# Kernel optimization log

Measured on AMD Instinct MI355X. Metric: run time of the kernel, lower is better.

Reference implementation:

```python
import jax, jax.numpy as jnp
import numpy as np

N_QUBITS = 8
N_LAYERS = 4


def _apply_1q(state, U, q):
    """Apply a 2x2 gate U (shape (2,2) shared, or (B,2,2) per-sample) on qubit q.
    state: (B, 2, 2, ..., 2) with qubit q on axis q+1 (wire 0 = most significant)."""
    a = q + 1
    st = jnp.moveaxis(state, a, -1)
    shp = st.shape
    st = st.reshape(shp[0], -1, 2)  # (B, rest, 2)
    if U.ndim == 3:
        st = jnp.einsum('bij,brj->bri', U, st)
    else:
        st = jnp.einsum('ij,brj->bri', U, st)
    return jnp.moveaxis(st.reshape(shp), -1, a)


def _cnot(state, c, t):
    ac, at = c + 1, t + 1
    s0 = jnp.take(state, 0, axis=ac)
    s1 = jnp.take(state, 1, axis=ac)
    at2 = at - 1 if at > ac else at  # axis shift after removing control axis
    s1 = jnp.flip(s1, axis=at2)      # X on target where control = 1
    return jnp.stack([s0, s1], axis=ac)


def _rx(t):
    c = jnp.cos(t / 2)
    s = jnp.sin(t / 2)
    return jnp.stack([jnp.stack([c + 0j, -1j * s]),
                      jnp.stack([-1j * s, c + 0j])]).astype(jnp.complex64)


def _ry(t):
    c = jnp.cos(t / 2)
    s = jnp.sin(t / 2)
    return jnp.stack([jnp.stack([c, -s]),
                      jnp.stack([s, c])]).astype(jnp.complex64)


def _rz(t):
    return jnp.diag(jnp.stack([jnp.exp(-1j * t / 2),
                               jnp.exp(1j * t / 2)])).astype(jnp.complex64)


def _ry_batched(t):
    # t: (B,) -> (B, 2, 2)
    c = jnp.cos(t / 2)
    s = jnp.sin(t / 2)
    U = jnp.stack([jnp.stack([c, -s], axis=-1),
                   jnp.stack([s, c], axis=-1)], axis=-2)
    return U.astype(jnp.complex64)


def setup_inputs() -> dict:
    key = jax.random.key(0)
    k1, k2 = jax.random.split(key)
    B = 16384
    x = jax.random.normal(k1, (B, N_QUBITS), dtype=jnp.float32)
    weights = jax.random.normal(k2, (N_QUBITS * N_LAYERS * 3,), dtype=jnp.float32) * 0.1
    return {"x": x, "weights": weights}


def reference(x, weights):
    n, L = N_QUBITS, N_LAYERS
    B = x.shape[0]
    state = jnp.zeros((B,) + (2,) * n, dtype=jnp.complex64)
    state = state.at[(slice(None),) + (0,) * n].set(1.0)

    # angle encoding: per-sample RY on each wire
    for q in range(n):
        state = _apply_1q(state, _ry_batched(x[:, q]), q)

    idx = 0
    for _ in range(L):
        for q in range(n):
            state = _apply_1q(state, _rx(weights[idx]), q)
            state = _apply_1q(state, _ry(weights[idx + 1]), q)
            state = _apply_1q(state, _rz(weights[idx + 2]), q)
            idx += 3
        for q in range(n - 1):
            state = _cnot(state, q, q + 1)

    p = jnp.abs(state) ** 2  # (B, 2, ..., 2) float32
    outs = []
    for q in range(n):
        axes = tuple(a for a in range(1, n + 1) if a != q + 1)
        z = p.sum(axis=axes)  # (B, 2)
        outs.append(z[:, 0] - z[:, 1])
    return jnp.stack(outs, axis=-1).astype(jnp.float32)
```

## Files before the change

### kernel.cpp

```cpp
#include <hip/hip_runtime.h>


#define NGATES 32

constexpr bool selon(int l, int d) {
    return (l == 0) ? (d == 0) : (((d + l - 1) & (l - 1)) == (l - 1));
}
constexpr int lm_of(int l, int q) {
    int m = 0;
    for (int d = 0; q + d <= 7; ++d)
        if ((l & d) == d) { int qq = q + d; if (qq <= 3) m |= 1 << (3 - qq); }
    return m;
}
constexpr int rm_of(int l, int q) {
    int m = 0;
    for (int d = 0; q + d <= 7; ++d)
        if ((l & d) == d) { int qq = q + d; if (qq >= 4) m |= 1 << (7 - qq); }
    return m;
}
constexpr int slm_of(int l, int q) {
    int m = 0;
    for (int d = 0; d <= q; ++d)
        if (selon(l, d)) { int k = q - d; if (k <= 3) m |= 1 << (3 - k); }
    return m;
}
constexpr int srm_of(int l, int q) {
    int m = 0;
    for (int d = 0; d <= q; ++d)
        if (selon(l, d)) { int k = q - d; if (k >= 4) m |= 1 << (7 - k); }
    return m;
}

__device__ __forceinline__ float xsgn(float f, unsigned m) {
    return __int_as_float(__float_as_int(f) ^ (int)m);
}

template<int C>
__device__ __forceinline__ int dppmov(int x) {
    return __builtin_amdgcn_update_dpp(x, x, C, 0xF, 0xF, false);
}
template<int M>
__device__ __forceinline__ float shx_dpp(float v) {
    int x = __float_as_int(v);
    if constexpr (M == 1)       { x = dppmov<0xB1>(x); }
    else if constexpr (M == 2)  { x = dppmov<0x4E>(x); }
    else if constexpr (M == 3)  { x = dppmov<0x1B>(x); }
    else if constexpr (M == 7)  { x = dppmov<0x141>(x); }
    else if constexpr (M == 8)  { x = dppmov<0x128>(x); }
    else                        { x = dppmov<0x140>(x); }
    return __int_as_float(x);
}
template<int M>
__device__ __forceinline__ float shx_ds(float v) {
    return __int_as_float(__builtin_amdgcn_ds_swizzle(__float_as_int(v), (M << 10) | 0x1F));
}
constexpr bool sgl(int M) {
    return M == 1 || M == 2 || M == 3 || M == 7 || M == 8 || M == 15;
}
template<int M>
__device__ __forceinline__ float shxm(float v) {
    if constexpr (sgl(M)) return shx_dpp<M>(v);
    else                  return shx_ds<M>(v);
}

template<int LM, int RM, int SLM, int SRM>
__device__ __forceinline__ void apply_gate(float ar[16], float ai[16], int lane,
                                           const float4 g)
{
    unsigned sm = 0;
    if constexpr (SLM != 0)
        sm = (unsigned)((__builtin_popcount(lane & SLM) & 1) << 31);
    const float c0r = g.x, c1i = g.w;
    const float c0i0 = xsgn(g.y, sm);
    const float c1r0 = xsgn(g.z, sm);
    const float c0i1 = xsgn(g.y, sm ^ 0x80000000u);
    const float c1r1 = xsgn(g.z, sm ^ 0x80000000u);

    float br[16], bi[16];
    #pragma unroll
    for (int r = 0; r < 16; ++r) {
        float pr = ar[r ^ RM], pi = ai[r ^ RM];
        if constexpr (LM != 0) { pr = shxm<LM>(pr); pi = shxm<LM>(pi); }
        br[r] = pr; bi[r] = pi;
    }
    #pragma unroll
    for (int r = 0; r < 16; ++r) {
        const bool c1 = (__builtin_popcount(r & SRM) & 1) != 0;
        const float c0i = c1 ? c0i1 : c0i0;
        const float c1r = c1 ? c1r1 : c1r0;
        const float nr = c0r*ar[r] - c0i*ai[r] + c1r*br[r] - c1i*bi[r];
        const float ni = c0r*ai[r] + c0i*ar[r] + c1r*bi[r] + c1i*br[r];
        ar[r] = nr; ai[r] = ni;
    }
}

#define GATE(L, Q) apply_gate<lm_of(L,Q), rm_of(L,Q), slm_of(L,Q), srm_of(L,Q)>( \
                       ar, ai, lane, gsh4[(L)*8+(Q)])
#define LAYER(L) GATE(L,0); GATE(L,1); GATE(L,2); GATE(L,3); \
                 GATE(L,4); GATE(L,5); GATE(L,6); GATE(L,7);

__global__ __launch_bounds__(256, 4) void qsim(const float* __restrict__ x,
                                               const float* __restrict__ w,
                                               float* __restrict__ out, int B)
{
    __shared__ float4 gsh4[NGATES];

    const int tid = threadIdx.x;
    if (tid < NGATES) {
        float hx = 0.5f * w[tid*3+0];
        float hy = 0.5f * w[tid*3+1];
        float hz = 0.5f * w[tid*3+2];
        float cx = cosf(hx), sx = sinf(hx);
        float cy = cosf(hy), sy = sinf(hy);
        float cz = cosf(hz), sz = sinf(hz);
        float m00r = cy*cx,  m00i =  sy*sx;
        float m01r = -sy*cx, m01i = -cy*sx;
        gsh4[tid] = make_float4(cz*m00r + sz*m00i,
                                cz*m00i - sz*m00r,
                                cz*m01r + sz*m01i,
                                cz*m01i - sz*m01r);
    }
    __syncthreads();

    const int lane = tid & 63;
    const int il   = lane & 15;
    const int sample = blockIdx.x * 16 + (tid >> 4);
    if (sample >= B) return;

    const float4* xp = (const float4*)(x + sample * 8);
    float4 xa = xp[0], xb = xp[1];
    float xs[8] = {xa.x, xa.y, xa.z, xa.w, xb.x, xb.y, xb.z, xb.w};
    float arf[8], aif[8], brf[8], bif[8];
    #pragma unroll
    for (int q = 0; q < 8; ++q) {
        float c, s;
        __sincosf(0.5f * xs[q], &s, &c);
        const float4 g = gsh4[q];
        arf[q] = g.x*c + g.z*s;
        aif[q] = g.y*c + g.w*s;
        brf[q] = g.x*s - g.z*c;
        bif[q] = g.w*c - g.y*s;
    }
    float Fr = (il & 8) ? brf[0] : arf[0];
    float Fi = (il & 8) ? bif[0] : aif[0];
    #pragma unroll
    for (int q = 1; q < 4; ++q) {
        const int bit = il & (8 >> q);
        const float gr = bit ? brf[q] : arf[q];
        const float gi = bit ? bif[q] : aif[q];
        const float nr = Fr*gr - Fi*gi;
        const float ni = Fr*gi + Fi*gr;
        Fr = nr; Fi = ni;
    }
    float t67r[4], t67i[4];
    #pragma unroll
    for (int b6 = 0; b6 < 2; ++b6)
        #pragma unroll
        for (int b7 = 0; b7 < 2; ++b7) {
            const float x6r = b6 ? brf[6] : arf[6], x6i = b6 ? bif[6] : aif[6];
            const float x7r = b7 ? brf[7] : arf[7], x7i = b7 ? bif[7] : aif[7];
            t67r[b6*2+b7] = x6r*x7r - x6i*x7i;
            t67i[b6*2+b7] = x6r*x7i + x6i*x7r;
        }
    float v57r[8], v57i[8];
    #pragma unroll
    for (int b5 = 0; b5 < 2; ++b5) {
        const float x5r = b5 ? brf[5] : arf[5], x5i = b5 ? bif[5] : aif[5];
        #pragma unroll
        for (int k = 0; k < 4; ++k) {
            v57r[b5*4+k] = x5r*t67r[k] - x5i*t67i[k];
            v57i[b5*4+k] = x5r*t67i[k] + x5i*t67r[k];
        }
    }
    float b4r[2], b4i[2];
    #pragma unroll
    for (int b4 = 0; b4 < 2; ++b4) {
        const float x4r = b4 ? brf[4] : arf[4], x4i = b4 ? bif[4] : aif[4];
        b4r[b4] = x4r*Fr - x4i*Fi;
        b4i[b4] = x4r*Fi + x4i*Fr;
    }
    float ar[16], ai[16];
    #pragma unroll
    for (int r = 0; r < 16; ++r) {
        const int hi = (r >> 3) & 1, lo = r & 7;
        ar[r] = b4r[hi]*v57r[lo] - b4i[hi]*v57i[lo];
        ai[r] = b4r[hi]*v57i[lo] + b4i[hi]*v57r[lo];
    }

    LAYER(1)
    LAYER(2)
    LAYER(3)

    float p[16];
    #pragma unroll
    for (int r = 0; r < 16; ++r) p[r] = ar[r]*ar[r] + ai[r]*ai[r];

    float s0[8], d0[8];
    #pragma unroll
    for (int k = 0; k < 8; ++k) { s0[k] = p[2*k] + p[2*k+1]; d0[k] = p[2*k] - p[2*k+1]; }
    float A0 = ((d0[0]+d0[1]) + (d0[2]+d0[3])) + ((d0[4]+d0[5]) + (d0[6]+d0[7]));
    float s1[4], d1[4];
    #pragma unroll
    for (int k = 0; k < 4; ++k) { s1[k] = s0[2*k] + s0[2*k+1]; d1[k] = s0[2*k] - s0[2*k+1]; }
    float A1 = (d1[0]+d1[1]) + (d1[2]+d1[3]);
    float s2[2], d2[2];
    #pragma unroll
    for (int k = 0; k < 2; ++k) { s2[k] = s1[2*k] + s1[2*k+1]; d2[k] = s1[2*k] - s1[2*k+1]; }
    float A2 = d2[0] + d2[1];
    float A3 = s2[0] - s2[1];
    float P  = s2[0] + s2[1];

    const unsigned sg1 = (unsigned)(il & 1) << 31;
    const unsigned sg2 = (unsigned)(il & 2) << 30;
    const unsigned sg4 = (unsigned)(il & 4) << 29;
    const unsigned sg8 = (unsigned)(il & 8) << 28;

    float wP = P;
    { float t = shxm<1>(wP); wP = t + xsgn(wP, sg1); }
    { float t = shxm<2>(wP); wP = t + xsgn(wP, sg2); }
    { float t = shxm<4>(wP); wP = t + xsgn(wP, sg4); }
    { float t = shxm<8>(wP); wP = t + xsgn(wP, sg8); }

    float a3 = xsgn(A3, sg8);
    a3 += shxm<1>(a3); a3 += shxm<2>(a3); a3 += shxm<4>(a3); a3 += shxm<8>(a3);
    float a2 = xsgn(A2, sg4);
    a2 += shxm<1>(a2); a2 += shxm<2>(a2); a2 += shxm<4>(a2); a2 += shxm<8>(a2);
    float a1 = xsgn(A1, sg2);
    a1 += shxm<1>(a1); a1 += shxm<2>(a1); a1 += shxm<4>(a1); a1 += shxm<8>(a1);
    float a0 = xsgn(A0, sg1);
    a0 += shxm<1>(a0); a0 += shxm<2>(a0); a0 += shxm<4>(a0); a0 += shxm<8>(a0);

    float* op = out + sample * 8;
    if (il == 8)      { op[0] = wP; op[4] = a3; }
    else if (il == 4) { op[1] = wP; op[5] = a2; }
    else if (il == 2) { op[2] = wP; op[6] = a1; }
    else if (il == 1) { op[3] = wP; op[7] = a0; }
}

extern "C" void kernel_launch(void* const* d_in, const int* in_sizes, int n_in,
                              void* d_out, int out_size, void* d_ws, size_t ws_size,
                              hipStream_t stream) {
    const float* x = (const float*)d_in[0];
    const float* w = (const float*)d_in[1];
    float* out = (float*)d_out;
    const int B = in_sizes[0] / 8;
    const int blocks = (B + 15) / 16;
    qsim<<<blocks, 256, 0, stream>>>(x, w, out, B);
}
```

Baseline: 80.35 us.

## Precompute layers 1-3 unitary and apply via FP16 MFMA complex GEMM

A first kernel builds the 256x256 unitary of layers 1-3 by simulating each basis state and stores it in fp16 in the workspace. A second kernel forms each sample's product state (encoding plus layer 0), multiplies it by the unitary with 16x16x32 fp16 MFMA complex matmuls, and reduces the Z expectations. This replaces per-sample gate-by-gate shuffle work with dense matrix-core throughput. The cost is an extra launch, fp16 precision loss in both the state and the unitary, far more FLOPs per sample, and low occupancy from heavy LDS use.

Result: slower. 102.9 us (+28.1%).

```diff
diff --git a/kernel.cpp b/kernel.cpp
--- a/kernel.cpp
+++ b/kernel.cpp
@@ -1,5 +1,9 @@
 #include <hip/hip_runtime.h>
 
+
+typedef _Float16 f16;
+typedef _Float16 h8_t __attribute__((ext_vector_type(8)));
+typedef float f4_t __attribute__((ext_vector_type(4)));
 
 #define NGATES 32
 
@@ -99,142 +103,238 @@
 #define LAYER(L) GATE(L,0); GATE(L,1); GATE(L,2); GATE(L,3); \
                  GATE(L,4); GATE(L,5); GATE(L,6); GATE(L,7);
 
-__global__ __launch_bounds__(256, 4) void qsim(const float* __restrict__ x,
-                                               const float* __restrict__ w,
-                                               float* __restrict__ out, int B)
+__device__ __forceinline__ float4 gate_row0(const float* w, int g) {
+    float hx = 0.5f * w[g*3+0];
+    float hy = 0.5f * w[g*3+1];
+    float hz = 0.5f * w[g*3+2];
+    float cx = cosf(hx), sx = sinf(hx);
+    float cy = cosf(hy), sy = sinf(hy);
+    float cz = cosf(hz), sz = sinf(hz);
+    float m00r = cy*cx,  m00i =  sy*sx;
+    float m01r = -sy*cx, m01i = -cy*sx;
+    return make_float4(cz*m00r + sz*m00i,
+                       cz*m00i - sz*m00r,
+                       cz*m01r + sz*m01i,
+                       cz*m01i - sz*m01r);
+}
+
+__global__ __launch_bounds__(256, 4) void build_u(const float* __restrict__ w,
+                                                  f16* __restrict__ bt_r,
+                                                  f16* __restrict__ bt_i)
 {
     __shared__ float4 gsh4[NGATES];
-
     const int tid = threadIdx.x;
-    if (tid < NGATES) {
-        float hx = 0.5f * w[tid*3+0];
-        float hy = 0.5f * w[tid*3+1];
-        float hz = 0.5f * w[tid*3+2];
-        float cx = cosf(hx), sx = sinf(hx);
-        float cy = cosf(hy), sy = sinf(hy);
-        float cz = cosf(hz), sz = sinf(hz);
-        float m00r = cy*cx,  m00i =  sy*sx;
-        float m01r = -sy*cx, m01i = -cy*sx;
-        gsh4[tid] = make_float4(cz*m00r + sz*m00i,
-                                cz*m00i - sz*m00r,
-                                cz*m01r + sz*m01i,
-                                cz*m01i - sz*m01r);
-    }
+    if (tid < NGATES) gsh4[tid] = gate_row0(w, tid);
     __syncthreads();
 
     const int lane = tid & 63;
     const int il   = lane & 15;
-    const int sample = blockIdx.x * 16 + (tid >> 4);
-    if (sample >= B) return;
-
-    const float4* xp = (const float4*)(x + sample * 8);
-    float4 xa = xp[0], xb = xp[1];
-    float xs[8] = {xa.x, xa.y, xa.z, xa.w, xb.x, xb.y, xb.z, xb.w};
-    float arf[8], aif[8], brf[8], bif[8];
-    #pragma unroll
-    for (int q = 0; q < 8; ++q) {
-        float c, s;
-        __sincosf(0.5f * xs[q], &s, &c);
-        const float4 g = gsh4[q];
-        arf[q] = g.x*c + g.z*s;
-        aif[q] = g.y*c + g.w*s;
-        brf[q] = g.x*s - g.z*c;
-        bif[q] = g.w*c - g.y*s;
-    }
-    float Fr = (il & 8) ? brf[0] : arf[0];
-    float Fi = (il & 8) ? bif[0] : aif[0];
-    #pragma unroll
-    for (int q = 1; q < 4; ++q) {
-        const int bit = il & (8 >> q);
-        const float gr = bit ? brf[q] : arf[q];
-        const float gi = bit ? bif[q] : aif[q];
-        const float nr = Fr*gr - Fi*gi;
-        const float ni = Fr*gi + Fi*gr;
-        Fr = nr; Fi = ni;
-    }
-    float t67r[4], t67i[4];
-    #pragma unroll
-    for (int b6 = 0; b6 < 2; ++b6)
-        #pragma unroll
-        for (int b7 = 0; b7 < 2; ++b7) {
-            const float x6r = b6 ? brf[6] : arf[6], x6i = b6 ? bif[6] : aif[6];
-            const float x7r = b7 ? brf[7] : arf[7], x7i = b7 ? bif[7] : aif[7];
-            t67r[b6*2+b7] = x6r*x7r - x6i*x7i;
-            t67i[b6*2+b7] = x6r*x7i + x6i*x7r;
-        }
-    float v57r[8], v57i[8];
-    #pragma unroll
-    for (int b5 = 0; b5 < 2; ++b5) {
-        const float x5r = b5 ? brf[5] : arf[5], x5i = b5 ? bif[5] : aif[5];
-        #pragma unroll
-        for (int k = 0; k < 4; ++k) {
-            v57r[b5*4+k] = x5r*t67r[k] - x5i*t67i[k];
-            v57i[b5*4+k] = x5r*t67i[k] + x5i*t67r[k];
-        }
-    }
-    float b4r[2], b4i[2];
-    #pragma unroll
-    for (int b4 = 0; b4 < 2; ++b4) {
-        const float x4r = b4 ? brf[4] : arf[4], x4i = b4 ? bif[4] : aif[4];
-        b4r[b4] = x4r*Fr - x4i*Fi;
-        b4i[b4] = x4r*Fi + x4i*Fr;
-    }
+    const int j    = blockIdx.x * 16 + (tid >> 4);
+
     float ar[16], ai[16];
     #pragma unroll
     for (int r = 0; r < 16; ++r) {
-        const int hi = (r >> 3) & 1, lo = r & 7;
-        ar[r] = b4r[hi]*v57r[lo] - b4i[hi]*v57i[lo];
-        ai[r] = b4r[hi]*v57i[lo] + b4i[hi]*v57r[lo];
-    }
-
+        ar[r] = (il == (j >> 4) && r == (j & 15)) ? 1.f : 0.f;
+        ai[r] = 0.f;
+    }
     LAYER(1)
     LAYER(2)
     LAYER(3)
-
-    float p[16];
-    #pragma unroll
-    for (int r = 0; r < 16; ++r) p[r] = ar[r]*ar[r] + ai[r]*ai[r];
-
-    float s0[8], d0[8];
-    #pragma unroll
-    for (int k = 0; k < 8; ++k) { s0[k] = p[2*k] + p[2*k+1]; d0[k] = p[2*k] - p[2*k+1]; }
-    float A0 = ((d0[0]+d0[1]) + (d0[2]+d0[3])) + ((d0[4]+d0[5]) + (d0[6]+d0[7]));
-    float s1[4], d1[4];
-    #pragma unroll
-    for (int k = 0; k < 4; ++k) { s1[k] = s0[2*k] + s0[2*k+1]; d1[k] = s0[2*k] - s0[2*k+1]; }
-    float A1 = (d1[0]+d1[1]) + (d1[2]+d1[3]);
-    float s2[2], d2[2];
-    #pragma unroll
-    for (int k = 0; k < 2; ++k) { s2[k] = s1[2*k] + s1[2*k+1]; d2[k] = s1[2*k] - s1[2*k+1]; }
-    float A2 = d2[0] + d2[1];
-    float A3 = s2[0] - s2[1];
-    float P  = s2[0] + s2[1];
-
-    const unsigned sg1 = (unsigned)(il & 1) << 31;
-    const unsigned sg2 = (unsigned)(il & 2) << 30;
-    const unsigned sg4 = (unsigned)(il & 4) << 29;
-    const unsigned sg8 = (unsigned)(il & 8) << 28;
-
-    float wP = P;
-    { float t = shxm<1>(wP); wP = t + xsgn(wP, sg1); }
-    { float t = shxm<2>(wP); wP = t + xsgn(wP, sg2); }
-    { float t = shxm<4>(wP); wP = t + xsgn(wP, sg4); }
-    { float t = shxm<8>(wP); wP = t + xsgn(wP, sg8); }
-
-    float a3 = xsgn(A3, sg8);
-    a3 += shxm<1>(a3); a3 += shxm<2>(a3); a3 += shxm<4>(a3); a3 += shxm<8>(a3);
-    float a2 = xsgn(A2, sg4);
-    a2 += shxm<1>(a2); a2 += shxm<2>(a2); a2 += shxm<4>(a2); a2 += shxm<8>(a2);
-    float a1 = xsgn(A1, sg2);
-    a1 += shxm<1>(a1); a1 += shxm<2>(a1); a1 += shxm<4>(a1); a1 += shxm<8>(a1);
-    float a0 = xsgn(A0, sg1);
-    a0 += shxm<1>(a0); a0 += shxm<2>(a0); a0 += shxm<4>(a0); a0 += shxm<8>(a0);
-
-    float* op = out + sample * 8;
-    if (il == 8)      { op[0] = wP; op[4] = a3; }
-    else if (il == 4) { op[1] = wP; op[5] = a2; }
-    else if (il == 2) { op[2] = wP; op[6] = a1; }
-    else if (il == 1) { op[3] = wP; op[7] = a0; }
+    #pragma unroll
+    for (int r = 0; r < 16; ++r) {
+        const int i = il * 16 + r;
+        bt_r[i * 256 + j] = (f16)ar[r];
+        bt_i[i * 256 + j] = (f16)ai[r];
+    }
+}
+
+struct cpx { float r, i; };
+__device__ __forceinline__ cpx cmul(cpx a, cpx b) {
+    return { a.r*b.r - a.i*b.i, a.r*b.i + a.i*b.r };
+}
+
+__device__ __forceinline__ f4_t mfma16(h8_t a, h8_t b, f4_t c) {
+    return __builtin_amdgcn_mfma_f32_16x16x32_f16(a, b, c, 0, 0, 0);
+}
+
+__global__ __launch_bounds__(256, 1) void qsim_mm(const float* __restrict__ x,
+                                                  const float* __restrict__ w,
+                                                  const f16* __restrict__ bt_r,
+                                                  const f16* __restrict__ bt_i,
+                                                  float* __restrict__ out)
+{
+    __shared__ f16  As_r[64][264], As_i[64][264];
+    __shared__ f16  BL_r[256][40], BL_i[256][40];
+    __shared__ float4 g0[8];
+    __shared__ float zbuf[4][64][8];
+
+    const int tid  = threadIdx.x;
+    const int lane = tid & 63;
+    const int wv   = tid >> 6;
+    const int lg   = (lane >> 4) & 3;
+    const int col  = lane & 15;
+
+    if (tid < 8) g0[tid] = gate_row0(w, tid);
+    __syncthreads();
+
+    {
+        const int sl = tid >> 2, pt = tid & 3;
+        const float4* xp = (const float4*)(x + (blockIdx.x * 64 + sl) * 8);
+        float4 xa = xp[0], xb = xp[1];
+        float xs[8] = {xa.x, xa.y, xa.z, xa.w, xb.x, xb.y, xb.z, xb.w};
+        cpx f0[8], f1[8];
+        #pragma unroll
+        for (int q = 0; q < 8; ++q) {
+            float c, s;
+            __sincosf(0.5f * xs[q], &s, &c);
+            const float4 g = g0[q];
+            f0[q] = { g.x*c + g.z*s, g.y*c + g.w*s };
+            f1[q] = { g.x*s - g.z*c, g.w*c - g.y*s };
+        }
+        cpx t01[4], t23[4], t45[4], t67[4];
+        #pragma unroll
+        for (int a = 0; a < 2; ++a)
+            #pragma unroll
+            for (int b = 0; b < 2; ++b) {
+                t01[a*2+b] = cmul(a ? f1[0] : f0[0], b ? f1[1] : f0[1]);
+                t23[a*2+b] = cmul(a ? f1[2] : f0[2], b ? f1[3] : f0[3]);
+                t45[a*2+b] = cmul(a ? f1[4] : f0[4], b ? f1[5] : f0[5]);
+                t67[a*2+b] = cmul(a ? f1[6] : f0[6], b ? f1[7] : f0[7]);
+            }
+        cpx P03[16], P47[16];
+        #pragma unroll
+        for (int h = 0; h < 16; ++h) {
+            P03[h] = cmul(t01[h >> 2], t23[h & 3]);
+            P47[h] = cmul(t45[h >> 2], t67[h & 3]);
+        }
+        #pragma unroll
+        for (int c8 = 0; c8 < 8; ++c8) {
+            const int j0 = pt * 64 + c8 * 8;
+            const int hi = j0 >> 4, lo0 = j0 & 15;
+            h8_t vr, vi;
+            #pragma unroll
+            for (int e = 0; e < 8; ++e) {
+                cpx cc = cmul(P03[hi], P47[lo0 + e]);
+                vr[e] = (f16)cc.r; vi[e] = (f16)cc.i;
+            }
+            *(h8_t*)&As_r[sl][j0] = vr;
+            *(h8_t*)&As_i[sl][j0] = vi;
+        }
+    }
+    {
+        const f16* sr = bt_r + tid * 256;
+        const f16* si = bt_i + tid * 256;
+        #pragma unroll
+        for (int c = 0; c < 4; ++c) {
+            *(h8_t*)&BL_r[tid][c*8] = *(const h8_t*)(sr + c*8);
+            *(h8_t*)&BL_i[tid][c*8] = *(const h8_t*)(si + c*8);
+        }
+    }
+    __syncthreads();
+
+    f4_t accr[4][4], acci[4][4];
+    #pragma unroll
+    for (int m = 0; m < 4; ++m)
+        #pragma unroll
+        for (int t = 0; t < 4; ++t) {
+            accr[m][t] = (f4_t){0.f,0.f,0.f,0.f};
+            acci[m][t] = (f4_t){0.f,0.f,0.f,0.f};
+        }
+
+    for (int ks = 0; ks < 8; ++ks) {
+        h8_t Ar[4], Ai[4];
+        #pragma unroll
+        for (int m = 0; m < 4; ++m) {
+            Ar[m] = *(const h8_t*)&As_r[m*16 + col][ks*32 + lg*8];
+            Ai[m] = *(const h8_t*)&As_i[m*16 + col][ks*32 + lg*8];
+        }
+        #pragma unroll
+        for (int t = 0; t < 4; ++t) {
+            const int n = (wv*4 + t) * 16 + col;
+            h8_t Br  = *(const h8_t*)&BL_r[n][lg*8];
+            h8_t Bi  = *(const h8_t*)&BL_i[n][lg*8];
+            h8_t nBi = -Bi;
+            #pragma unroll
+            for (int m = 0; m < 4; ++m) {
+                accr[m][t] = mfma16(Ar[m], Br,  accr[m][t]);
+                accr[m][t] = mfma16(Ai[m], nBi, accr[m][t]);
+                acci[m][t] = mfma16(Ar[m], Bi,  acci[m][t]);
+                acci[m][t] = mfma16(Ai[m], Br,  acci[m][t]);
+            }
+        }
+        __syncthreads();
+        if (ks < 7) {
+            const f16* sr = bt_r + tid * 256 + (ks+1) * 32;
+            const f16* si = bt_i + tid * 256 + (ks+1) * 32;
+            #pragma unroll
+            for (int c = 0; c < 4; ++c) {
+                *(h8_t*)&BL_r[tid][c*8] = *(const h8_t*)(sr + c*8);
+                *(h8_t*)&BL_i[tid][c*8] = *(const h8_t*)(si + c*8);
+            }
+            __syncthreads();
+        }
+    }
+
+    constexpr int RM8[8] = {0x80, 0x40, 0x20, 0x10, 0x88, 0x44, 0x22, 0x11};
+    float sgl_[8];
+    #pragma unroll
+    for (int q = 0; q < 8; ++q)
+        sgl_[q] = (__builtin_popcount(col & (RM8[q] & 15)) & 1) ? -1.f : 1.f;
+
+    float z[4][4][8];
+    #pragma unroll
+    for (int m = 0; m < 4; ++m)
+        #pragma unroll
+        for (int v = 0; v < 4; ++v)
+            #pragma unroll
+            for (int q = 0; q < 8; ++q) z[m][v][q] = 0.f;
+
+    #pragma unroll
+    for (int t = 0; t < 4; ++t) {
+        const int nt = wv*4 + t;
+        float sgf[8];
+        #pragma unroll
+        for (int q = 0; q < 8; ++q)
+            sgf[q] = (__builtin_popcount(nt & (RM8[q] >> 4)) & 1) ? -sgl_[q] : sgl_[q];
+        #pragma unroll
+        for (int m = 0; m < 4; ++m)
+            #pragma unroll
+            for (int v = 0; v < 4; ++v) {
+                const float p = accr[m][t][v]*accr[m][t][v]
+                              + acci[m][t][v]*acci[m][t][v];
+                #pragma unroll
+                for (int q = 0; q < 8; ++q)
+                    z[m][v][q] = fmaf(sgf[q], p, z[m][v][q]);
+            }
+    }
+    #pragma unroll
+    for (int m = 0; m < 4; ++m)
+        #pragma unroll
+        for (int v = 0; v < 4; ++v)
+            #pragma unroll
+            for (int q = 0; q < 8; ++q) {
+                float r = z[m][v][q];
+                r += shxm<1>(r); r += shxm<2>(r);
+                r += shxm<4>(r); r += shxm<8>(r);
+                z[m][v][q] = r;
+            }
+    #pragma unroll
+    for (int q = 0; q < 8; ++q)
+        if (col == q) {
+            #pragma unroll
+            for (int m = 0; m < 4; ++m)
+                #pragma unroll
+                for (int v = 0; v < 4; ++v)
+                    zbuf[wv][m*16 + lg*4 + v][q] = z[m][v][q];
+        }
+    __syncthreads();
+    #pragma unroll
+    for (int k = 0; k < 2; ++k) {
+        const int slot = tid * 2 + k;
+        const int s = slot >> 3, q = slot & 7;
+        out[(blockIdx.x * 64 + s) * 8 + q] =
+            zbuf[0][s][q] + zbuf[1][s][q] + zbuf[2][s][q] + zbuf[3][s][q];
+    }
 }
 
 extern "C" void kernel_launch(void* const* d_in, const int* in_sizes, int n_in,
@@ -244,6 +344,8 @@
     const float* w = (const float*)d_in[1];
     float* out = (float*)d_out;
     const int B = in_sizes[0] / 8;
-    const int blocks = (B + 15) / 16;
-    qsim<<<blocks, 256, 0, stream>>>(x, w, out, B);
-}
+    f16* bt_r = (f16*)d_ws;
+    f16* bt_i = bt_r + 256 * 256;
+    build_u<<<16, 256, 0, stream>>>(w, bt_r, bt_i);
+    qsim_mm<<<(B + 63) / 64, 256, 0, stream>>>(x, w, bt_r, bt_i, out);
+}
```
